# Optimization experiments

Hardware: AMD Instinct MI355X
Metric: run time of the kernel (lower is better)

The kernel has to match this reference:

```python
import jax, jax.numpy as jnp
import numpy as np

N = 50000      # nodes
E = 800000     # edges (before self-loops)
G = 128        # graphs in batch
IN = 128       # in_channels
HID = 32       # hidden_channels (per head)
HEADS = 4
OUT = 64       # out_channels
SLOPE = 0.2    # PyG GATConv default negative_slope


def setup_inputs() -> dict:
    key = jax.random.key(0)
    ks = jax.random.split(key, 24)
    s = 0.1
    inp = {
        'x': jax.random.normal(ks[0], (N, IN), jnp.float32),
        'edge_index': jax.random.randint(ks[1], (2, E), 0, N, dtype=jnp.int32),
        'batch': jnp.sort(jax.random.randint(ks[2], (N,), 0, G, dtype=jnp.int32)),
        # conv1: IN -> HEADS*HID, concat
        'W1': jax.random.normal(ks[3], (IN, HEADS * HID), jnp.float32) * s,
        'a1s': jax.random.normal(ks[4], (HEADS, HID), jnp.float32) * s,
        'a1d': jax.random.normal(ks[5], (HEADS, HID), jnp.float32) * s,
        'b1': jnp.zeros((HEADS * HID,), jnp.float32),
        # conv2: HEADS*HID -> HEADS*HID, concat
        'W2': jax.random.normal(ks[6], (HEADS * HID, HEADS * HID), jnp.float32) * s,
        'a2s': jax.random.normal(ks[7], (HEADS, HID), jnp.float32) * s,
        'a2d': jax.random.normal(ks[8], (HEADS, HID), jnp.float32) * s,
        'b2': jnp.zeros((HEADS * HID,), jnp.float32),
        # conv3
        'W3': jax.random.normal(ks[9], (HEADS * HID, HEADS * HID), jnp.float32) * s,
        'a3s': jax.random.normal(ks[10], (HEADS, HID), jnp.float32) * s,
        'a3d': jax.random.normal(ks[11], (HEADS, HID), jnp.float32) * s,
        'b3': jnp.zeros((HEADS * HID,), jnp.float32),
        # conv4: heads=1, concat=False -> HID
        'W4': jax.random.normal(ks[12], (HEADS * HID, 1 * HID), jnp.float32) * s,
        'a4s': jax.random.normal(ks[13], (1, HID), jnp.float32) * s,
        'a4d': jax.random.normal(ks[14], (1, HID), jnp.float32) * s,
        'b4': jnp.zeros((HID,), jnp.float32),
        # fc: HID -> OUT
        'fcW': jax.random.normal(ks[15], (HID, OUT), jnp.float32) * s,
        'fcb': jnp.zeros((OUT,), jnp.float32),
    }
    return inp


def gat_conv(x, src, dst, W, a_src, a_dst, bias, heads, ch, concat):
    # x: [N, F_in]; src/dst: [E'] with self-loops (PyG add_self_loops=True)
    h = (x @ W).reshape(N, heads, ch)                       # [N, H, C]
    alpha_s = jnp.einsum('nhc,hc->nh', h, a_src)            # [N, H]
    alpha_d = jnp.einsum('nhc,hc->nh', h, a_dst)
    e = jax.nn.leaky_relu(alpha_s[src] + alpha_d[dst], SLOPE)  # [E', H]
    # segment softmax over edges grouped by destination node
    e_max = jax.ops.segment_max(e, dst, num_segments=N)
    e = jnp.exp(e - e_max[dst])
    denom = jax.ops.segment_sum(e, dst, num_segments=N)
    alpha = e / (denom[dst] + 1e-16)                        # [E', H]
    msg = h[src] * alpha[:, :, None]                        # [E', H, C]
    out = jax.ops.segment_sum(msg, dst, num_segments=N)     # [N, H, C]
    out = out.reshape(N, heads * ch) if concat else out.mean(axis=1)
    return out + bias


def reference(x, edge_index, batch, W1, a1s, a1d, b1, W2, a2s, a2d, b2,
              W3, a3s, a3d, b3, W4, a4s, a4d, b4, fcW, fcb):
    loop = jnp.arange(N, dtype=edge_index.dtype)
    src = jnp.concatenate([edge_index[0], loop])            # add self-loops once
    dst = jnp.concatenate([edge_index[1], loop])
    h = jax.nn.elu(gat_conv(x, src, dst, W1, a1s, a1d, b1, HEADS, HID, True))
    h = jax.nn.elu(gat_conv(h, src, dst, W2, a2s, a2d, b2, HEADS, HID, True))
    h = jax.nn.elu(gat_conv(h, src, dst, W3, a3s, a3d, b3, HEADS, HID, True))
    h = jax.nn.elu(gat_conv(h, src, dst, W4, a4s, a4d, b4, 1, HID, False))
    # global mean pool over graphs
    counts = jax.ops.segment_sum(jnp.ones((N,), h.dtype), batch, num_segments=G)
    pooled = jax.ops.segment_sum(h, batch, num_segments=G) / jnp.maximum(counts, 1.0)[:, None]
    # dropout p=0.5 is identity at inference
    return pooled @ fcW + fcb                               # [G, OUT]
```

## Files before the change

### kernel.cpp

```cpp
#include <hip/hip_runtime.h>
#include <hip/hip_bf16.h>


constexpr int NN     = 50000;
constexpr int NNPAD  = 50048;
constexpr int EE     = 800000;
constexpr int ETOT   = EE + NN;
constexpr int GG     = 128;
constexpr int HIDC   = 32;
constexpr int OUTC   = 64;

constexpr int NRANGE = (NN + 127) / 128;
constexpr int EPB    = 4096;
constexpr int NBLK   = (EE + EPB - 1) / EPB;
constexpr int RCAP   = 2688;

typedef short  bf16x8 __attribute__((ext_vector_type(8)));
typedef float  f32x4  __attribute__((ext_vector_type(4)));

static __device__ __forceinline__ unsigned short f2bf(float f) {
    __hip_bfloat16 h = __float2bfloat16(f);
    unsigned short u; __builtin_memcpy(&u, &h, 2); return u;
}
static __device__ __forceinline__ unsigned int f2bf2(float lo, float hi) {
    __hip_bfloat162 h2 = __float22bfloat162_rn(make_float2(lo, hi));
    unsigned int u; __builtin_memcpy(&u, &h2, 4); return u;
}
static __device__ __forceinline__ float bflo(unsigned int v) {
    return __uint_as_float(v << 16);
}
static __device__ __forceinline__ float bfhi(unsigned int v) {
    return __uint_as_float(v & 0xffff0000u);
}
static __device__ __forceinline__ float elu(float v) {
    return (v > 0.f) ? v : (__expf(v) - 1.f);
}
static __device__ __forceinline__ float leaky(float e) {
    return fmaxf(e, 0.f) + 0.2f * fminf(e, 0.f);
}

__global__ __launch_bounds__(256) void local_sort_kernel(
    const int* __restrict__ ei,
    unsigned int* __restrict__ blocksorted,
    int* __restrict__ boffs)
{
    __shared__ unsigned int sorted[EPB];
    __shared__ int hist[NRANGE + 1];
    __shared__ int scanv[NRANGE + 1];
    __shared__ int cur[NRANGE + 1];
    __shared__ int wsum4[4];
    __shared__ int ct_s;

    const int b = blockIdx.x, tid = threadIdx.x;
    const int lane = tid & 63, wid = tid >> 6;
    const int e0 = b * EPB;
    const int ecnt = min(EPB, EE - e0);

    for (int t = tid; t < NRANGE + 1; t += 256) hist[t] = 0;
    __syncthreads();

    unsigned int recs[16];
    int rkey[16];
#pragma unroll
    for (int k = 0; k < 16; ++k) {
        const int idx = tid + k * 256;
        rkey[k] = -1;
        if (idx < ecnt) {
            const int src = ei[e0 + idx];
            const int dst = ei[EE + e0 + idx];
            const int r = dst >> 7;
            recs[k] = (unsigned int)src | ((unsigned int)(dst & 127) << 16);
            rkey[k] = r;
            atomicAdd(&hist[r], 1);
        }
    }
    __syncthreads();

    int carry = 0;
    for (int base = 0; base < NRANGE + 1; base += 256) {
        const int i = base + tid;
        const int v = (i < NRANGE + 1) ? hist[i] : 0;
        int incl = v;
#pragma unroll
        for (int off = 1; off < 64; off <<= 1) {
            int t = __shfl_up(incl, off, 64);
            if (lane >= off) incl += t;
        }
        if (lane == 63) wsum4[wid] = incl;
        __syncthreads();
        if (tid == 0) {
            int s = 0;
#pragma unroll
            for (int w = 0; w < 4; ++w) { int t = wsum4[w]; wsum4[w] = s; s += t; }
            ct_s = s;
        }
        __syncthreads();
        const int excl = carry + wsum4[wid] + incl - v;
        if (i < NRANGE + 1) { scanv[i] = excl; cur[i] = excl; }
        carry += ct_s;
        __syncthreads();
    }

#pragma unroll
    for (int k = 0; k < 16; ++k) {
        if (rkey[k] >= 0) {
            const int pos = atomicAdd(&cur[rkey[k]], 1);
            sorted[pos] = recs[k];
        }
    }
    __syncthreads();

    for (int t = tid; t < ecnt; t += 256)
        blocksorted[(size_t)b * EPB + t] = sorted[t];
    for (int t = tid; t < NRANGE + 1; t += 256)
        boffs[b * (NRANGE + 1) + t] = scanv[t];
}

__global__ __launch_bounds__(256) void rtot_kernel(const int* __restrict__ boffs,
                                                   int* __restrict__ rtot)
{
    const int r = blockIdx.x * 4 + (threadIdx.x >> 6);
    const int lane = threadIdx.x & 63;
    if (r >= NRANGE) return;
    int tot = 0;
    for (int b = lane; b < NBLK; b += 64) {
        const int* bp = boffs + b * (NRANGE + 1) + r;
        tot += bp[1] - bp[0];
    }
#pragma unroll
    for (int k = 1; k < 64; k <<= 1) tot += __shfl_xor(tot, k, 64);
    if (lane == 0) rtot[r] = tot + min(128, NN - r * 128);
}

__global__ __launch_bounds__(512) void rscan_kernel(const int* __restrict__ rtot,
                                                    int* __restrict__ rbase)
{
    __shared__ int wsum[8], wpre[8];
    const int tid = threadIdx.x, lane = tid & 63, wid = tid >> 6;
    int tot = (tid < NRANGE) ? rtot[tid] : 0;
    int incl = tot;
#pragma unroll
    for (int off = 1; off < 64; off <<= 1) {
        int t = __shfl_up(incl, off, 64);
        if (lane >= off) incl += t;
    }
    if (lane == 63) wsum[wid] = incl;
    __syncthreads();
    if (tid < 8) {
        int wv = wsum[tid], winc = wv;
#pragma unroll
        for (int off = 1; off < 8; off <<= 1) {
            int t = __shfl_up(winc, off, 64);
            if (tid >= off) winc += t;
        }
        wpre[tid] = winc - wv;
    }
    __syncthreads();
    const int excl = wpre[wid] + incl - tot;
    if (tid < NRANGE) rbase[tid] = excl;
    if (tid == NRANGE - 1) rbase[NRANGE] = excl + tot;
}

__global__ __launch_bounds__(256) void phaseB_kernel(
    const int* __restrict__ boffs,
    const unsigned int* __restrict__ blocksorted,
    const int* __restrict__ rbase,
    int* __restrict__ offs,
    unsigned int* __restrict__ csrpack)
{
    __shared__ unsigned int rec[RCAP];
    __shared__ unsigned int outpk[RCAP];
    __shared__ int runoff[NBLK + 1];
    __shared__ int bstart[NBLK];
    __shared__ int hist[128], lofs[128], cur[128];
    __shared__ int wsum4[4];
    __shared__ int tot0_s;

    const int r = blockIdx.x, tid = threadIdx.x;
    const int lane = tid & 63, wid = tid >> 6;
    const int base = r * 128;
    const int rn   = min(128, NN - base);

    int cnt = 0;
    if (tid < NBLK) {
        const int* bp = boffs + tid * (NRANGE + 1) + r;
        const int s = bp[0];
        bstart[tid] = s;
        cnt = bp[1] - s;
    }
    if (tid < 128) hist[tid] = 0;
    int incl = cnt;
#pragma unroll
    for (int off = 1; off < 64; off <<= 1) {
        int t = __shfl_up(incl, off, 64);
        if (lane >= off) incl += t;
    }
    if (lane == 63) wsum4[wid] = incl;
    __syncthreads();
    if (tid == 0) {
        int s = 0;
#pragma unroll
        for (int w = 0; w < 4; ++w) { int t = wsum4[w]; wsum4[w] = s; s += t; }
    }
    __syncthreads();
    const int excl = wsum4[wid] + incl - cnt;
    if (tid <= NBLK) runoff[tid] = excl;
    __syncthreads();

    const int tot8 = runoff[NBLK];
    for (int i = tid; i < tot8; i += 256) {
        int lo = 0, hi = NBLK;
        while (lo + 1 < hi) {
            const int mid = (lo + hi) >> 1;
            if (runoff[mid] <= i) lo = mid; else hi = mid;
        }
        rec[i] = blocksorted[(size_t)lo * EPB + bstart[lo] + (i - runoff[lo])];
    }
    for (int t = tid; t < rn; t += 256)
        rec[tot8 + t] = (unsigned int)(base + t) | ((unsigned int)t << 16);
    const int total = min(tot8 + rn, RCAP);
    __syncthreads();

    for (int t = tid; t < total; t += 256) atomicAdd(&hist[rec[t] >> 16], 1);
    __syncthreads();

    if (tid < 64) {
        int v = hist[tid], incl2 = v;
#pragma unroll
        for (int off = 1; off < 64; off <<= 1) {
            int t = __shfl_up(incl2, off, 64);
            if (tid >= off) incl2 += t;
        }
        lofs[tid] = incl2 - v;
        if (tid == 63) tot0_s = incl2;
    }
    __syncthreads();
    if (tid >= 64 && tid < 128) {
        const int l = tid & 63;
        int v = hist[tid], incl2 = v;
#pragma unroll
        for (int off = 1; off < 64; off <<= 1) {
            int t = __shfl_up(incl2, off, 64);
            if (l >= off) incl2 += t;
        }
        lofs[tid] = tot0_s + incl2 - v;
    }
    __syncthreads();

    if (tid < 128) cur[tid] = lofs[tid];
    if (tid < rn) offs[base + tid] = rbase[r] + lofs[tid];
    if (r == 0 && tid == 0) offs[NN] = rbase[NRANGE];
    __syncthreads();

    for (int t = tid; t < total; t += 256) {
        const unsigned int rc = rec[t];
        const int pos = atomicAdd(&cur[rc >> 16], 1);
        outpk[pos] = (rc & 0xffffu) | ((unsigned int)(base + (rc >> 16)) << 16);
    }
    __syncthreads();
    const int rb = rbase[r];
    for (int t = tid; t < total; t += 256) csrpack[rb + t] = outpk[t];
}

__global__ __launch_bounds__(256) void prep_kernel(
    const float* __restrict__ W1, const float* __restrict__ a1s, const float* __restrict__ a1d,
    const float* __restrict__ W2, const float* __restrict__ a2s, const float* __restrict__ a2d,
    const float* __restrict__ W3, const float* __restrict__ a3s, const float* __restrict__ a3d,
    const float* __restrict__ W4, const float* __restrict__ a4s, const float* __restrict__ a4d,
    unsigned short* __restrict__ wtg)
{
    __shared__ float ahat_s[128 * 8];
    const int l = blockIdx.x, tid = threadIdx.x;
    const float *W, *as_, *ad_;
    int fo, nh;
    if (l == 0)      { W = W1; as_ = a1s; ad_ = a1d; fo = 128; nh = 4; }
    else if (l == 1) { W = W2; as_ = a2s; ad_ = a2d; fo = 128; nh = 4; }
    else if (l == 2) { W = W3; as_ = a3s; ad_ = a3d; fo = 128; nh = 4; }
    else             { W = W4; as_ = a4s; ad_ = a4d; fo = 32;  nh = 1; }
    const int F_STG = fo + 16;

    for (int item = tid; item < 128 * 8; item += 256) {
        const int k = item >> 3, j = item & 7;
        const int hh = j & 3;
        const bool is_d = j >= 4;
        float v = 0.f;
        if (hh < nh) {
            const float* av = (is_d ? ad_ : as_) + hh * 32;
            const float* wp = W + (size_t)k * fo + hh * 32;
#pragma unroll 8
            for (int c = 0; c < 32; ++c) v = fmaf(wp[c], av[c], v);
        }
        ahat_s[item] = v;
    }
    __syncthreads();

    unsigned short* outb = wtg + (size_t)l * (144 * 128);
    for (int p = tid; p < F_STG * 64; p += 256) {
        const int n  = p % F_STG;
        const int k2 = p / F_STG;
        float w0 = 0.f, w1 = 0.f;
        if (n < fo) {
            w0 = W[(size_t)(2 * k2) * fo + n];
            w1 = W[(size_t)(2 * k2 + 1) * fo + n];
        } else {
            const int j = n - fo;
            if (j < 8) {
                w0 = ahat_s[(2 * k2) * 8 + j];
                w1 = ahat_s[(2 * k2 + 1) * 8 + j];
            }
        }
        const unsigned int packed = f2bf2(w0, w1);
        const int byte = n * 256 + ((4 * k2) ^ ((n & 7) << 4));
        *reinterpret_cast<unsigned int*>(reinterpret_cast<char*>(outb) + byte) = packed;
    }
}

template<int F_OUT, int NH, bool XF32>
__global__ __launch_bounds__(256) void gemm_mfma_kernel(
    const void* __restrict__ xv,
    const unsigned short* __restrict__ wtg,
    unsigned short* __restrict__ hb,
    float* __restrict__ as_out, float* __restrict__ ad_out)
{
    constexpr int F_STG = F_OUT + 16;
    __shared__ unsigned short wt[F_STG * 128];
    const int tid = threadIdx.x;

    {
        const bf16x8* __restrict__ wg = reinterpret_cast<const bf16x8*>(wtg);
        bf16x8* wl = reinterpret_cast<bf16x8*>(wt);
        constexpr int NV = F_STG * 16;
#pragma unroll
        for (int i = 0; i < NV / 256; ++i)
            wl[i * 256 + tid] = wg[i * 256 + tid];
    }
    __syncthreads();

    const int wave = tid >> 6, lane = tid & 63;
    const int kchunk = (lane >> 4) * 8;
    const int kb_base = (lane >> 4) * 16;

#pragma unroll
    for (int rr = 0; rr < 2; ++rr) {
        const int row0 = blockIdx.x * 128 + rr * 64 + wave * 16;
        const int arow = row0 + (lane & 15);

        bf16x8 a[4];
        if (XF32) {
            if (arow < NN) {
                const float* __restrict__ ap = (const float*)xv + (size_t)arow * 128;
#pragma unroll
                for (int ks = 0; ks < 4; ++ks) {
                    const float4 f0 = *reinterpret_cast<const float4*>(ap + ks * 32 + kchunk);
                    const float4 f1 = *reinterpret_cast<const float4*>(ap + ks * 32 + kchunk + 4);
                    uint4 u;
                    u.x = f2bf2(f0.x, f0.y);
                    u.y = f2bf2(f0.z, f0.w);
                    u.z = f2bf2(f1.x, f1.y);
                    u.w = f2bf2(f1.z, f1.w);
                    bf16x8 v; __builtin_memcpy(&v, &u, 16);
                    a[ks] = v;
                }
            } else {
#pragma unroll
                for (int ks = 0; ks < 4; ++ks) a[ks] = bf16x8{0,0,0,0,0,0,0,0};
            }
        } else {
            const unsigned short* __restrict__ ap =
                (const unsigned short*)xv + (size_t)arow * 128;
#pragma unroll
            for (int ks = 0; ks < 4; ++ks)
                a[ks] = *reinterpret_cast<const bf16x8*>(ap + ks * 32 + kchunk);
        }

        const int rbase = row0 + (lane >> 4) * 4;

#pragma unroll
        for (int nt = 0; nt < F_OUT / 16; ++nt) {
            const int n = nt * 16 + (lane & 15);
            f32x4 acc = {0.f, 0.f, 0.f, 0.f};
#pragma unroll
            for (int ks = 0; ks < 4; ++ks) {
                const int byte = n * 256 + ((ks * 64 + kb_base) ^ ((n & 7) << 4));
                bf16x8 b = *reinterpret_cast<const bf16x8*>(
                    reinterpret_cast<const char*>(wt) + byte);
                acc = __builtin_amdgcn_mfma_f32_16x16x32_bf16(a[ks], b, acc, 0, 0, 0);
            }
#pragma unroll
            for (int r = 0; r < 4; ++r) {
                const int row = rbase + r;
                if (row < NN)
                    hb[(size_t)row * F_OUT + n] = f2bf(acc[r]);
            }
        }

        {
            const int n = F_OUT + (lane & 15);
            f32x4 acc = {0.f, 0.f, 0.f, 0.f};
#pragma unroll
            for (int ks = 0; ks < 4; ++ks) {
                const int byte = n * 256 + ((ks * 64 + kb_base) ^ ((n & 7) << 4));
                bf16x8 b = *reinterpret_cast<const bf16x8*>(
                    reinterpret_cast<const char*>(wt) + byte);
                acc = __builtin_amdgcn_mfma_f32_16x16x32_bf16(a[ks], b, acc, 0, 0, 0);
            }
            const int col = lane & 15;
            if (col < 8) {
                const int hh = col & 3;
                const bool is_d = col >= 4;
                if (hh < NH) {
                    float* op = is_d ? ad_out : as_out;
#pragma unroll
                    for (int r = 0; r < 4; ++r) {
                        const int row = rbase + r;
                        if (row < NN) {
                            if (NH == 4) op[row * 4 + hh] = acc[r];
                            else         op[row]          = acc[r];
                        }
                    }
                }
            }
        }
    }
}

template<int HEADS, int F_OUT, bool OUT_BF16>
__global__ __launch_bounds__(256) void aggregate_kernel(
    const unsigned short* __restrict__ hlin,
    const float* __restrict__ as_,
    const float* __restrict__ ad_,
    const int* __restrict__ offs,
    const unsigned int* __restrict__ csrpack,
    const float* __restrict__ bias,
    void* __restrict__ out_v)
{
    __shared__ float w_all[4][64 * HEADS];
    __shared__ int   s_all[4][64];
    const int wave = threadIdx.x >> 6;
    const int lane = threadIdx.x & 63;
    const int d    = blockIdx.x * 4 + wave;
    if (d >= NN) return;
    float* __restrict__ w_lds   = w_all[wave];
    int*   __restrict__ src_lds = s_all[wave];

    const int beg = offs[d], end = offs[d + 1];

    float ad_h[HEADS];
#pragma unroll
    for (int h = 0; h < HEADS; ++h) ad_h[h] = ad_[d * HEADS + h];

    float acc[8] = {0.f, 0.f, 0.f, 0.f, 0.f, 0.f, 0.f, 0.f};
    float dsum = 0.f;
    const int q  = (F_OUT == 128) ? (lane >> 4) : (lane >> 2);
    const int cl = (F_OUT == 128) ? (lane & 15) : (lane & 3);
    const int hd = (F_OUT == 128) ? (cl >> 2) : 0;

    for (int base = beg; base < end; base += 64) {
        const int cnt = min(64, end - base);
        {
            const int p = base + lane;
            const unsigned int pk = (p < end) ? csrpack[p] : 0u;
            const int src = (int)(pk & 0xffffu);
            src_lds[lane] = src;
            if (HEADS == 4) {
                float4 w4 = make_float4(0.f, 0.f, 0.f, 0.f);
                if (p < end) {
                    const float4 s4 = *reinterpret_cast<const float4*>(
                        as_ + (size_t)src * 4);
                    w4.x = __expf(leaky(s4.x + ad_h[0]));
                    w4.y = __expf(leaky(s4.y + ad_h[1]));
                    w4.z = __expf(leaky(s4.z + ad_h[2]));
                    w4.w = __expf(leaky(s4.w + ad_h[3]));
                }
                *reinterpret_cast<float4*>(w_lds + lane * 4) = w4;
            } else {
                float w1 = 0.f;
                if (p < end) w1 = __expf(leaky(as_[src] + ad_h[0]));
                w_lds[lane] = w1;
            }
        }
        asm volatile("s_waitcnt lgkmcnt(0)" ::: "memory");

        if (F_OUT == 128) {
            const int cntR = (cnt + 3) & ~3;
#pragma unroll 4
            for (int j = 0; j < cntR; j += 4) {
                const int   slot = j + q;
                const int   srcj = src_lds[slot];
                const float w    = w_lds[slot * 4 + hd];
                const uint4 hv   = *reinterpret_cast<const uint4*>(
                    hlin + (size_t)srcj * 128 + cl * 8);
                dsum += w;
                acc[0] = fmaf(w, bflo(hv.x), acc[0]);
                acc[1] = fmaf(w, bfhi(hv.x), acc[1]);
                acc[2] = fmaf(w, bflo(hv.y), acc[2]);
                acc[3] = fmaf(w, bfhi(hv.y), acc[3]);
                acc[4] = fmaf(w, bflo(hv.z), acc[4]);
                acc[5] = fmaf(w, bfhi(hv.z), acc[5]);
                acc[6] = fmaf(w, bflo(hv.w), acc[6]);
                acc[7] = fmaf(w, bfhi(hv.w), acc[7]);
            }
        } else {
            const int cntR = (cnt + 15) & ~15;
#pragma unroll 4
            for (int j = 0; j < cntR; j += 16) {
                const int   slot = j + q;
                const int   srcj = src_lds[slot];
                const float w    = w_lds[slot];
                const uint4 hv   = *reinterpret_cast<const uint4*>(
                    hlin + (size_t)srcj * 32 + cl * 8);
                dsum += w;
                acc[0] = fmaf(w, bflo(hv.x), acc[0]);
                acc[1] = fmaf(w, bfhi(hv.x), acc[1]);
                acc[2] = fmaf(w, bflo(hv.y), acc[2]);
                acc[3] = fmaf(w, bfhi(hv.y), acc[3]);
                acc[4] = fmaf(w, bflo(hv.z), acc[4]);
                acc[5] = fmaf(w, bfhi(hv.z), acc[5]);
                acc[6] = fmaf(w, bflo(hv.w), acc[6]);
                acc[7] = fmaf(w, bfhi(hv.w), acc[7]);
            }
        }
    }

    if (F_OUT == 128) {
#pragma unroll
        for (int t = 0; t < 8; ++t) {
            acc[t] += __shfl_xor(acc[t], 16, 64);
            acc[t] += __shfl_xor(acc[t], 32, 64);
        }
        dsum += __shfl_xor(dsum, 16, 64);
        dsum += __shfl_xor(dsum, 32, 64);
        if (lane < 16) {
            const float rinv = 1.f / (dsum + 1e-16f);
            const int c0 = lane * 8;
            float v[8];
#pragma unroll
            for (int t = 0; t < 8; ++t) v[t] = elu(fmaf(acc[t], rinv, bias[c0 + t]));
            uint4 pk;
            pk.x = f2bf2(v[0], v[1]);
            pk.y = f2bf2(v[2], v[3]);
            pk.z = f2bf2(v[4], v[5]);
            pk.w = f2bf2(v[6], v[7]);
            *reinterpret_cast<uint4*>((unsigned short*)out_v + (size_t)d * 128 + c0) = pk;
        }
    } else {
#pragma unroll
        for (int t = 0; t < 8; ++t) {
            acc[t] += __shfl_xor(acc[t], 4, 64);
            acc[t] += __shfl_xor(acc[t], 8, 64);
            acc[t] += __shfl_xor(acc[t], 16, 64);
            acc[t] += __shfl_xor(acc[t], 32, 64);
        }
        dsum += __shfl_xor(dsum, 4, 64);
        dsum += __shfl_xor(dsum, 8, 64);
        dsum += __shfl_xor(dsum, 16, 64);
        dsum += __shfl_xor(dsum, 32, 64);
        if (lane < 4) {
            const float rinv = 1.f / (dsum + 1e-16f);
            const int c0 = lane * 8;
            float v[8];
#pragma unroll
            for (int t = 0; t < 8; ++t) v[t] = elu(fmaf(acc[t], rinv, bias[c0 + t]));
            float* op = (float*)out_v + (size_t)d * 32 + c0;
            *reinterpret_cast<float4*>(op)     = make_float4(v[0], v[1], v[2], v[3]);
            *reinterpret_cast<float4*>(op + 4) = make_float4(v[4], v[5], v[6], v[7]);
        }
    }
}

__global__ __launch_bounds__(256) void pool_fc_kernel(
    const float* __restrict__ h4, const int* __restrict__ batch,
    const float* __restrict__ fcW, const float* __restrict__ fcb,
    float* __restrict__ out)
{
    const int g = blockIdx.x;
    __shared__ int sb, se;
    if (threadIdx.x == 0) {
        int lo = 0, hi = NN;
        while (lo < hi) { int mid = (lo + hi) >> 1; if (batch[mid] < g) lo = mid + 1; else hi = mid; }
        sb = lo;
        lo = sb; hi = NN;
        while (lo < hi) { int mid = (lo + hi) >> 1; if (batch[mid] < g + 1) lo = mid + 1; else hi = mid; }
        se = lo;
    }
    __syncthreads();
    const int s = sb, e = se;

    const int c  = threadIdx.x & 31;
    const int rg = threadIdx.x >> 5;
    float acc = 0.f;
    for (int n = s + rg; n < e; n += 8)
        acc += h4[(size_t)n * HIDC + c];

    __shared__ float red[8][32];
    red[rg][c] = acc;
    __syncthreads();
    __shared__ float pooled_s[32];
    if (threadIdx.x < 32) {
        float v = 0.f;
#pragma unroll
        for (int r = 0; r < 8; ++r) v += red[r][threadIdx.x];
        pooled_s[threadIdx.x] = v / fmaxf((float)(e - s), 1.f);
    }
    __syncthreads();
    if (threadIdx.x < OUTC) {
        const int o = threadIdx.x;
        float a2 = fcb[o];
#pragma unroll
        for (int cc = 0; cc < HIDC; ++cc)
            a2 = fmaf(pooled_s[cc], fcW[cc * OUTC + o], a2);
        out[g * OUTC + o] = a2;
    }
}

extern "C" void kernel_launch(void* const* d_in, const int* in_sizes, int n_in,
                              void* d_out, int out_size, void* d_ws, size_t ws_size,
                              hipStream_t stream)
{
    const float* x     = (const float*)d_in[0];
    const int*   ei    = (const int*)d_in[1];
    const int*   batch = (const int*)d_in[2];
    const float* W1  = (const float*)d_in[3];
    const float* a1s = (const float*)d_in[4];
    const float* a1d = (const float*)d_in[5];
    const float* b1  = (const float*)d_in[6];
    const float* W2  = (const float*)d_in[7];
    const float* a2s = (const float*)d_in[8];
    const float* a2d = (const float*)d_in[9];
    const float* b2  = (const float*)d_in[10];
    const float* W3  = (const float*)d_in[11];
    const float* a3s = (const float*)d_in[12];
    const float* a3d = (const float*)d_in[13];
    const float* b3  = (const float*)d_in[14];
    const float* W4  = (const float*)d_in[15];
    const float* a4s = (const float*)d_in[16];
    const float* a4d = (const float*)d_in[17];
    const float* b4  = (const float*)d_in[18];
    const float* fcW = (const float*)d_in[19];
    const float* fcb = (const float*)d_in[20];
    float* out = (float*)d_out;

    unsigned short* xb = (unsigned short*)d_ws;
    unsigned short* hb = xb + (size_t)NNPAD * 128;
    float* asb  = (float*)(hb + (size_t)NNPAD * 128);
    float* adb  = asb + (size_t)NN * 4;
    int*   offs    = (int*)(adb + (size_t)NN * 4);
    unsigned int* csrpack = (unsigned int*)(offs + NN + 1);
    int*   boffs  = (int*)(csrpack + ETOT);
    int*   rbase  = boffs + NBLK * (NRANGE + 1);
    int*   rtot   = rbase + NRANGE + 1;
    unsigned short* wtg = (unsigned short*)(rtot + NRANGE);
    unsigned int* blocksorted = (unsigned int*)hb;
    float* bufF = (float*)xb;

    local_sort_kernel<<<NBLK, 256, 0, stream>>>(ei, blocksorted, boffs);
    rtot_kernel<<<(NRANGE + 3) / 4, 256, 0, stream>>>(boffs, rtot);
    rscan_kernel<<<1, 512, 0, stream>>>(rtot, rbase);
    phaseB_kernel<<<NRANGE, 256, 0, stream>>>(boffs, blocksorted, rbase, offs, csrpack);

    prep_kernel<<<4, 256, 0, stream>>>(W1, a1s, a1d, W2, a2s, a2d,
                                       W3, a3s, a3d, W4, a4s, a4d, wtg);

    constexpr int GEMM_GRID = NNPAD / 128;
    constexpr int AGG_GRID  = (NN + 3) / 4;
    constexpr size_t WSTRIDE = 144 * 128;

    gemm_mfma_kernel<128, 4, true><<<GEMM_GRID, 256, 0, stream>>>(x, wtg + 0 * WSTRIDE, hb, asb, adb);
    aggregate_kernel<4, 128, true><<<AGG_GRID, 256, 0, stream>>>(hb, asb, adb, offs, csrpack, b1, xb);
    gemm_mfma_kernel<128, 4, false><<<GEMM_GRID, 256, 0, stream>>>(xb, wtg + 1 * WSTRIDE, hb, asb, adb);
    aggregate_kernel<4, 128, true><<<AGG_GRID, 256, 0, stream>>>(hb, asb, adb, offs, csrpack, b2, xb);
    gemm_mfma_kernel<128, 4, false><<<GEMM_GRID, 256, 0, stream>>>(xb, wtg + 2 * WSTRIDE, hb, asb, adb);
    aggregate_kernel<4, 128, true><<<AGG_GRID, 256, 0, stream>>>(hb, asb, adb, offs, csrpack, b3, xb);
    gemm_mfma_kernel<32, 1, false><<<GEMM_GRID, 256, 0, stream>>>(xb, wtg + 3 * WSTRIDE, hb, asb, adb);
    aggregate_kernel<1, 32, false><<<AGG_GRID, 256, 0, stream>>>(hb, asb, adb, offs, csrpack, b4, bufF);

    pool_fc_kernel<<<GG, 256, 0, stream>>>(bufF, batch, fcW, fcb, out);
}
```

Before: 258.1 us.

## Fuse edge local-sort with first-layer GEMM into one heterogeneous launch

```diff
diff --git a/kernel.cpp b/kernel.cpp
--- a/kernel.cpp
+++ b/kernel.cpp
@@ -39,19 +39,18 @@
     return fmaxf(e, 0.f) + 0.2f * fminf(e, 0.f);
 }
 
-__global__ __launch_bounds__(256) void local_sort_kernel(
-    const int* __restrict__ ei,
-    unsigned int* __restrict__ blocksorted,
-    int* __restrict__ boffs)
-{
-    __shared__ unsigned int sorted[EPB];
-    __shared__ int hist[NRANGE + 1];
-    __shared__ int scanv[NRANGE + 1];
-    __shared__ int cur[NRANGE + 1];
-    __shared__ int wsum4[4];
-    __shared__ int ct_s;
-
-    const int b = blockIdx.x, tid = threadIdx.x;
+static __device__ void local_sort_body(
+    char* smem, const int* __restrict__ ei,
+    unsigned int* __restrict__ blocksorted, int* __restrict__ boffs, int b)
+{
+    unsigned int* sorted = reinterpret_cast<unsigned int*>(smem);
+    int* hist  = reinterpret_cast<int*>(smem + EPB * 4);
+    int* scanv = hist + (NRANGE + 1);
+    int* cur   = scanv + (NRANGE + 1);
+    int* wsum4 = cur + (NRANGE + 1);
+    int* ct_s  = wsum4 + 4;
+
+    const int tid = threadIdx.x;
     const int lane = tid & 63, wid = tid >> 6;
     const int e0 = b * EPB;
     const int ecnt = min(EPB, EE - e0);
@@ -92,12 +91,12 @@
             int s = 0;
 #pragma unroll
             for (int w = 0; w < 4; ++w) { int t = wsum4[w]; wsum4[w] = s; s += t; }
-            ct_s = s;
+            *ct_s = s;
         }
         __syncthreads();
         const int excl = carry + wsum4[wid] + incl - v;
         if (i < NRANGE + 1) { scanv[i] = excl; cur[i] = excl; }
-        carry += ct_s;
+        carry += *ct_s;
         __syncthreads();
     }
 
@@ -114,6 +113,145 @@
         blocksorted[(size_t)b * EPB + t] = sorted[t];
     for (int t = tid; t < NRANGE + 1; t += 256)
         boffs[b * (NRANGE + 1) + t] = scanv[t];
+}
+
+template<int F_OUT, int NH, bool XF32>
+static __device__ void gemm_body(
+    char* smem, const void* __restrict__ xv,
+    const unsigned short* __restrict__ wtg,
+    unsigned short* __restrict__ hb,
+    float* __restrict__ as_out, float* __restrict__ ad_out, int bid)
+{
+    constexpr int F_STG = F_OUT + 16;
+    unsigned short* wt = reinterpret_cast<unsigned short*>(smem);
+    const int tid = threadIdx.x;
+
+    {
+        const bf16x8* __restrict__ wg = reinterpret_cast<const bf16x8*>(wtg);
+        bf16x8* wl = reinterpret_cast<bf16x8*>(wt);
+        constexpr int NV = F_STG * 16;
+#pragma unroll
+        for (int i = 0; i < NV / 256; ++i)
+            wl[i * 256 + tid] = wg[i * 256 + tid];
+    }
+    __syncthreads();
+
+    const int wave = tid >> 6, lane = tid & 63;
+    const int kchunk = (lane >> 4) * 8;
+    const int kb_base = (lane >> 4) * 16;
+
+#pragma unroll
+    for (int rr = 0; rr < 2; ++rr) {
+        const int row0 = bid * 128 + rr * 64 + wave * 16;
+        const int arow = row0 + (lane & 15);
+
+        bf16x8 a[4];
+        if (XF32) {
+            if (arow < NN) {
+                const float* __restrict__ ap = (const float*)xv + (size_t)arow * 128;
+#pragma unroll
+                for (int ks = 0; ks < 4; ++ks) {
+                    const float4 f0 = *reinterpret_cast<const float4*>(ap + ks * 32 + kchunk);
+                    const float4 f1 = *reinterpret_cast<const float4*>(ap + ks * 32 + kchunk + 4);
+                    uint4 u;
+                    u.x = f2bf2(f0.x, f0.y);
+                    u.y = f2bf2(f0.z, f0.w);
+                    u.z = f2bf2(f1.x, f1.y);
+                    u.w = f2bf2(f1.z, f1.w);
+                    bf16x8 v; __builtin_memcpy(&v, &u, 16);
+                    a[ks] = v;
+                }
+            } else {
+#pragma unroll
+                for (int ks = 0; ks < 4; ++ks) a[ks] = bf16x8{0,0,0,0,0,0,0,0};
+            }
+        } else {
+            const unsigned short* __restrict__ ap =
+                (const unsigned short*)xv + (size_t)arow * 128;
+#pragma unroll
+            for (int ks = 0; ks < 4; ++ks)
+                a[ks] = *reinterpret_cast<const bf16x8*>(ap + ks * 32 + kchunk);
+        }
+
+        const int rbase = row0 + (lane >> 4) * 4;
+
+#pragma unroll
+        for (int nt = 0; nt < F_OUT / 16; ++nt) {
+            const int n = nt * 16 + (lane & 15);
+            f32x4 acc = {0.f, 0.f, 0.f, 0.f};
+#pragma unroll
+            for (int ks = 0; ks < 4; ++ks) {
+                const int byte = n * 256 + ((ks * 64 + kb_base) ^ ((n & 7) << 4));
+                bf16x8 b = *reinterpret_cast<const bf16x8*>(
+                    reinterpret_cast<const char*>(wt) + byte);
+                acc = __builtin_amdgcn_mfma_f32_16x16x32_bf16(a[ks], b, acc, 0, 0, 0);
+            }
+#pragma unroll
+            for (int r = 0; r < 4; ++r) {
+                const int row = rbase + r;
+                if (row < NN)
+                    hb[(size_t)row * F_OUT + n] = f2bf(acc[r]);
+            }
+        }
+
+        {
+            const int n = F_OUT + (lane & 15);
+            f32x4 acc = {0.f, 0.f, 0.f, 0.f};
+#pragma unroll
+            for (int ks = 0; ks < 4; ++ks) {
+                const int byte = n * 256 + ((ks * 64 + kb_base) ^ ((n & 7) << 4));
+                bf16x8 b = *reinterpret_cast<const bf16x8*>(
+                    reinterpret_cast<const char*>(wt) + byte);
+                acc = __builtin_amdgcn_mfma_f32_16x16x32_bf16(a[ks], b, acc, 0, 0, 0);
+            }
+            const int col = lane & 15;
+            if (col < 8) {
+                const int hh = col & 3;
+                const bool is_d = col >= 4;
+                if (hh < NH) {
+                    float* op = is_d ? ad_out : as_out;
+#pragma unroll
+                    for (int r = 0; r < 4; ++r) {
+                        const int row = rbase + r;
+                        if (row < NN) {
+                            if (NH == 4) op[row * 4 + hh] = acc[r];
+                            else         op[row]          = acc[r];
+                        }
+                    }
+                }
+            }
+        }
+    }
+}
+
+constexpr int FUSED_SMEM = 144 * 128 * 2;
+
+__global__ __launch_bounds__(256) void fused_ls_gemm1_kernel(
+    const int* __restrict__ ei,
+    unsigned int* __restrict__ blocksorted,
+    int* __restrict__ boffs,
+    const float* __restrict__ x,
+    const unsigned short* __restrict__ wtg,
+    unsigned short* __restrict__ hb,
+    float* __restrict__ as_out, float* __restrict__ ad_out)
+{
+    __shared__ char smem[FUSED_SMEM];
+    if (blockIdx.x < NBLK)
+        local_sort_body(smem, ei, blocksorted, boffs, blockIdx.x);
+    else
+        gemm_body<128, 4, true>(smem, x, wtg, hb, as_out, ad_out,
+                                blockIdx.x - NBLK);
+}
+
+template<int F_OUT, int NH>
+__global__ __launch_bounds__(256) void gemm_mfma_kernel(
+    const void* __restrict__ xv,
+    const unsigned short* __restrict__ wtg,
+    unsigned short* __restrict__ hb,
+    float* __restrict__ as_out, float* __restrict__ ad_out)
+{
+    __shared__ char smem[(F_OUT + 16) * 128 * 2];
+    gemm_body<F_OUT, NH, false>(smem, xv, wtg, hb, as_out, ad_out, blockIdx.x);
 }
 
 __global__ __launch_bounds__(256) void rtot_kernel(const int* __restrict__ boffs,
@@ -312,115 +450,6 @@
         const unsigned int packed = f2bf2(w0, w1);
         const int byte = n * 256 + ((4 * k2) ^ ((n & 7) << 4));
         *reinterpret_cast<unsigned int*>(reinterpret_cast<char*>(outb) + byte) = packed;
-    }
-}
-
-template<int F_OUT, int NH, bool XF32>
-__global__ __launch_bounds__(256) void gemm_mfma_kernel(
-    const void* __restrict__ xv,
-    const unsigned short* __restrict__ wtg,
-    unsigned short* __restrict__ hb,
-    float* __restrict__ as_out, float* __restrict__ ad_out)
-{
-    constexpr int F_STG = F_OUT + 16;
-    __shared__ unsigned short wt[F_STG * 128];
-    const int tid = threadIdx.x;
-
-    {
-        const bf16x8* __restrict__ wg = reinterpret_cast<const bf16x8*>(wtg);
-        bf16x8* wl = reinterpret_cast<bf16x8*>(wt);
-        constexpr int NV = F_STG * 16;
-#pragma unroll
-        for (int i = 0; i < NV / 256; ++i)
-            wl[i * 256 + tid] = wg[i * 256 + tid];
-    }
-    __syncthreads();
-
-    const int wave = tid >> 6, lane = tid & 63;
-    const int kchunk = (lane >> 4) * 8;
-    const int kb_base = (lane >> 4) * 16;
-
-#pragma unroll
-    for (int rr = 0; rr < 2; ++rr) {
-        const int row0 = blockIdx.x * 128 + rr * 64 + wave * 16;
-        const int arow = row0 + (lane & 15);
-
-        bf16x8 a[4];
-        if (XF32) {
-            if (arow < NN) {
-                const float* __restrict__ ap = (const float*)xv + (size_t)arow * 128;
-#pragma unroll
-                for (int ks = 0; ks < 4; ++ks) {
-                    const float4 f0 = *reinterpret_cast<const float4*>(ap + ks * 32 + kchunk);
-                    const float4 f1 = *reinterpret_cast<const float4*>(ap + ks * 32 + kchunk + 4);
-                    uint4 u;
-                    u.x = f2bf2(f0.x, f0.y);
-                    u.y = f2bf2(f0.z, f0.w);
-                    u.z = f2bf2(f1.x, f1.y);
-                    u.w = f2bf2(f1.z, f1.w);
-                    bf16x8 v; __builtin_memcpy(&v, &u, 16);
-                    a[ks] = v;
-                }
-            } else {
-#pragma unroll
-                for (int ks = 0; ks < 4; ++ks) a[ks] = bf16x8{0,0,0,0,0,0,0,0};
-            }
-        } else {
-            const unsigned short* __restrict__ ap =
-                (const unsigned short*)xv + (size_t)arow * 128;
-#pragma unroll
-            for (int ks = 0; ks < 4; ++ks)
-                a[ks] = *reinterpret_cast<const bf16x8*>(ap + ks * 32 + kchunk);
-        }
-
-        const int rbase = row0 + (lane >> 4) * 4;
-
-#pragma unroll
-        for (int nt = 0; nt < F_OUT / 16; ++nt) {
-            const int n = nt * 16 + (lane & 15);
-            f32x4 acc = {0.f, 0.f, 0.f, 0.f};
-#pragma unroll
-            for (int ks = 0; ks < 4; ++ks) {
-                const int byte = n * 256 + ((ks * 64 + kb_base) ^ ((n & 7) << 4));
-                bf16x8 b = *reinterpret_cast<const bf16x8*>(
-                    reinterpret_cast<const char*>(wt) + byte);
-                acc = __builtin_amdgcn_mfma_f32_16x16x32_bf16(a[ks], b, acc, 0, 0, 0);
-            }
-#pragma unroll
-            for (int r = 0; r < 4; ++r) {
-                const int row = rbase + r;
-                if (row < NN)
-                    hb[(size_t)row * F_OUT + n] = f2bf(acc[r]);
-            }
-        }
-
-        {
-            const int n = F_OUT + (lane & 15);
-            f32x4 acc = {0.f, 0.f, 0.f, 0.f};
-#pragma unroll
-            for (int ks = 0; ks < 4; ++ks) {
-                const int byte = n * 256 + ((ks * 64 + kb_base) ^ ((n & 7) << 4));
-                bf16x8 b = *reinterpret_cast<const bf16x8*>(
-                    reinterpret_cast<const char*>(wt) + byte);
-                acc = __builtin_amdgcn_mfma_f32_16x16x32_bf16(a[ks], b, acc, 0, 0, 0);
-            }
-            const int col = lane & 15;
-            if (col < 8) {
-                const int hh = col & 3;
-                const bool is_d = col >= 4;
-                if (hh < NH) {
-                    float* op = is_d ? ad_out : as_out;
-#pragma unroll
-                    for (int r = 0; r < 4; ++r) {
-                        const int row = rbase + r;
-                        if (row < NN) {
-                            if (NH == 4) op[row * 4 + hh] = acc[r];
-                            else         op[row]          = acc[r];
-                        }
-                    }
-                }
-            }
-        }
     }
 }
 
@@ -483,7 +512,7 @@
 
         if (F_OUT == 128) {
             const int cntR = (cnt + 3) & ~3;
-#pragma unroll 4
+#pragma unroll 2
             for (int j = 0; j < cntR; j += 4) {
                 const int   slot = j + q;
                 const int   srcj = src_lds[slot];
@@ -502,7 +531,7 @@
             }
         } else {
             const int cntR = (cnt + 15) & ~15;
-#pragma unroll 4
+#pragma unroll 2
             for (int j = 0; j < cntR; j += 16) {
                 const int   slot = j + q;
                 const int   srcj = src_lds[slot];
@@ -650,28 +679,29 @@
     int*   rbase  = boffs + NBLK * (NRANGE + 1);
     int*   rtot   = rbase + NRANGE + 1;
     unsigned short* wtg = (unsigned short*)(rtot + NRANGE);
-    unsigned int* blocksorted = (unsigned int*)hb;
+    unsigned int* blocksorted = (unsigned int*)(wtg + 4 * 144 * 128);
     float* bufF = (float*)xb;
 
-    local_sort_kernel<<<NBLK, 256, 0, stream>>>(ei, blocksorted, boffs);
+    prep_kernel<<<4, 256, 0, stream>>>(W1, a1s, a1d, W2, a2s, a2d,
+                                       W3, a3s, a3d, W4, a4s, a4d, wtg);
+
+    constexpr int GEMM_GRID = NNPAD / 128;
+    constexpr int AGG_GRID  = (NN + 3) / 4;
+    constexpr size_t WSTRIDE = 144 * 128;
+
+    fused_ls_gemm1_kernel<<<NBLK + GEMM_GRID, 256, 0, stream>>>(
+        ei, blocksorted, boffs, x, wtg + 0 * WSTRIDE, hb, asb, adb);
+
     rtot_kernel<<<(NRANGE + 3) / 4, 256, 0, stream>>>(boffs, rtot);
     rscan_kernel<<<1, 512, 0, stream>>>(rtot, rbase);
     phaseB_kernel<<<NRANGE, 256, 0, stream>>>(boffs, blocksorted, rbase, offs, csrpack);
 
-    prep_kernel<<<4, 256, 0, stream>>>(W1, a1s, a1d, W2, a2s, a2d,
-                                       W3, a3s, a3d, W4, a4s, a4d, wtg);
-
-    constexpr int GEMM_GRID = NNPAD / 128;
-    constexpr int AGG_GRID  = (NN + 3) / 4;
-    constexpr size_t WSTRIDE = 144 * 128;
-
-    gemm_mfma_kernel<128, 4, true><<<GEMM_GRID, 256, 0, stream>>>(x, wtg + 0 * WSTRIDE, hb, asb, adb);
     aggregate_kernel<4, 128, true><<<AGG_GRID, 256, 0, stream>>>(hb, asb, adb, offs, csrpack, b1, xb);
-    gemm_mfma_kernel<128, 4, false><<<GEMM_GRID, 256, 0, stream>>>(xb, wtg + 1 * WSTRIDE, hb, asb, adb);
+    gemm_mfma_kernel<128, 4><<<GEMM_GRID, 256, 0, stream>>>(xb, wtg + 1 * WSTRIDE, hb, asb, adb);
     aggregate_kernel<4, 128, true><<<AGG_GRID, 256, 0, stream>>>(hb, asb, adb, offs, csrpack, b2, xb);
-    gemm_mfma_kernel<128, 4, false><<<GEMM_GRID, 256, 0, stream>>>(xb, wtg + 2 * WSTRIDE, hb, asb, adb);
+    gemm_mfma_kernel<128, 4><<<GEMM_GRID, 256, 0, stream>>>(xb, wtg + 2 * WSTRIDE, hb, asb, adb);
     aggregate_kernel<4, 128, true><<<AGG_GRID, 256, 0, stream>>>(hb, asb, adb, offs, csrpack, b3, xb);
-    gemm_mfma_kernel<32, 1, false><<<GEMM_GRID, 256, 0, stream>>>(xb, wtg + 3 * WSTRIDE, hb, asb, adb);
+    gemm_mfma_kernel<32, 1><<<GEMM_GRID, 256, 0, stream>>>(xb, wtg + 3 * WSTRIDE, hb, asb, adb);
     aggregate_kernel<1, 32, false><<<AGG_GRID, 256, 0, stream>>>(hb, asb, adb, offs, csrpack, b4, bufF);
 
     pool_fc_kernel<<<GG, 256, 0, stream>>>(bufF, batch, fcW, fcb, out);
```

Result: faster. 240.4 us (-6.9%).
